# Performance work log

Measured on AMD Instinct MI355X. Metric: run time of the kernel, lower is better.

The kernel has to match this reference:

```python
import jax, jax.numpy as jnp
import numpy as np

B, S, D, H = 2, 2048, 1024, 16
HD = D // H
EPS = 1e-8


def setup_inputs() -> dict:
    key = jax.random.key(0)
    ks = jax.random.split(key, 6)
    x = jax.random.normal(ks[0], (B, S, D), jnp.float32)
    V = jax.random.normal(ks[1], (B, S, H, HD), jnp.float32)
    # binary sparsity mask [B, S, S]
    M = (jax.random.uniform(ks[2], (B, S, S)) > 0.5).astype(jnp.float32)
    # packed QKV in-projection of nn.MultiheadAttention
    in_proj_w = jax.random.normal(ks[3], (3 * D, D), jnp.float32) / np.sqrt(D).astype(np.float32)
    in_proj_b = jnp.zeros((3 * D,), jnp.float32)
    # module-level out_proj (the mha's internal out_proj is discarded)
    out_w = jax.random.normal(ks[4], (D, D), jnp.float32) / np.sqrt(D).astype(np.float32)
    out_b = jnp.zeros((D,), jnp.float32)
    return dict(x=x, V=V, M=M, in_proj_w=in_proj_w, in_proj_b=in_proj_b,
                out_w=out_w, out_b=out_b)


def reference(x, V, M, in_proj_w, in_proj_b, out_w, out_b):
    b, s, d = x.shape
    # packed QKV projection (torch MHA semantics); v-proj computed but its
    # output path (mha output) is discarded by the module, so skip it.
    qkv = x @ in_proj_w.T + in_proj_b              # [B,S,3D]
    q, k, _ = jnp.split(qkv, 3, axis=-1)
    q = q.reshape(b, s, H, HD).transpose(0, 2, 1, 3)   # [B,H,S,HD]
    k = k.reshape(b, s, H, HD).transpose(0, 2, 1, 3)
    scale = np.float32(1.0 / np.sqrt(HD))
    scores = jnp.einsum('bhsd,bhtd->bhst', q, k) * scale  # [B,H,S,S]
    A = jax.nn.softmax(scores, axis=-1)
    # mask + L1 renormalization over keys
    A_sparse = A * M[:, None, :, :]
    norm = jnp.sum(jnp.abs(A_sparse), axis=-1, keepdims=True) + EPS
    A_bar = A_sparse / norm
    # separate value tensor V: [B,S,H,HD] -> [B,H,S,HD]
    Vp = V.transpose(0, 2, 1, 3)
    out = jnp.einsum('bhst,bhtd->bhsd', A_bar, Vp)  # [B,H,S,HD]
    out = out.transpose(0, 2, 1, 3).reshape(b, s, d)
    return out @ out_w.T + out_b
```

## Files before the change

### kernel.cpp

```cpp
#include <hip/hip_runtime.h>
#include <hip/hip_bf16.h>

#define B_  2
#define S_  2048
#define D_  1024
#define H_  16
#define HD_ 64

using bf16x8  = __attribute__((ext_vector_type(8))) __bf16;
using floatx4 = __attribute__((ext_vector_type(4))) float;
using intx4   = __attribute__((ext_vector_type(4))) int;

__device__ __forceinline__ unsigned short f2bf(float f) {
  union { float f; unsigned int i; } v; v.f = f;
  unsigned int r = v.i + 0x7fffu + ((v.i >> 16) & 1u);
  return (unsigned short)(r >> 16);
}
__device__ __forceinline__ unsigned int f2bf_pk(float a, float b) {
  union { __hip_bfloat162 h2; unsigned int u; } c;
  c.h2 = __float22bfloat162_rn(make_float2(a, b));
  return c.u;
}
__device__ __forceinline__ floatx4 mfma16(bf16x8 a, bf16x8 b, floatx4 c) {
  return __builtin_amdgcn_mfma_f32_16x16x32_bf16(a, b, c, 0, 0, 0);
}
__device__ __forceinline__ void gld16(const unsigned short* g, unsigned short* l) {
  __builtin_amdgcn_global_load_lds(
      (const __attribute__((address_space(1))) unsigned int*)g,
      (__attribute__((address_space(3))) unsigned int*)l, 16, 0, 0);
}
#define SW8(row, g) ((((g) ^ ((row) & 7)) * 8))
#define SW4(row, g) ((((g) ^ (((row) >> 1) & 3)) * 8))
#define TAU(r) (((r) & 0x23) | (((r) & 0x08) << 1) | (((r) & 0x04) << 1) | (((r) & 0x10) >> 2))

__global__ __launch_bounds__(256) void prep_kernel(
    const float* __restrict__ x, const float* __restrict__ w_in,
    const float* __restrict__ w_out, const float* __restrict__ V,
    const float* __restrict__ Mm,
    unsigned short* __restrict__ xb, unsigned short* __restrict__ wb,
    unsigned short* __restrict__ wob, unsigned short* __restrict__ vt,
    unsigned long long* __restrict__ mpk)
{
  __shared__ unsigned short tile[64 * 72];
  const int bid = blockIdx.x, tid = threadIdx.x;

  if (bid < 3584) {
    const float* src; unsigned short* dst; int base;
    if (bid < 2048)      { src = x;     dst = xb;  base = bid; }
    else if (bid < 3072) { src = w_in;  dst = wb;  base = bid - 2048; }
    else                 { src = w_out; dst = wob; base = bid - 3072; }
    const int i = (base * 256 + tid) * 8;
    float4 a = *(const float4*)(src + i);
    float4 b = *(const float4*)(src + i + 4);
    union { unsigned int w[4]; intx4 v; } o;
    o.w[0] = f2bf_pk(a.x, a.y); o.w[1] = f2bf_pk(a.z, a.w);
    o.w[2] = f2bf_pk(b.x, b.y); o.w[3] = f2bf_pk(b.z, b.w);
    *(intx4*)(dst + i) = o.v;
  } else if (bid < 5632) {
    const int wave = tid >> 6, lane = tid & 63;
    const int w0 = (bid - 3584) * 64 + wave * 16;
#pragma unroll 4
    for (int j = 0; j < 16; ++j) {
      float v = Mm[(size_t)(w0 + j) * 64 + lane];
      unsigned long long bl = __ballot(v != 0.0f);
      if (lane == 0) mpk[w0 + j] = bl;
    }
  } else {
    const int idx = bid - 5632;
    const int t0 = (idx & 31) * 64, h = (idx >> 5) & 15, b = idx >> 9;
    const int sr = tid >> 3, sc = (tid & 7) * 8;
    const float* src = V + ((size_t)((b * S_ + t0) * H_ + h)) * HD_;
#pragma unroll
    for (int half = 0; half < 2; ++half) {
      const int r = sr + half * 32;
      float4 v0 = *(const float4*)&src[(size_t)r * (H_ * HD_) + sc];
      float4 v1 = *(const float4*)&src[(size_t)r * (H_ * HD_) + sc + 4];
      union { unsigned int w[4]; intx4 v; } p;
      p.w[0] = f2bf_pk(v0.x, v0.y); p.w[1] = f2bf_pk(v0.z, v0.w);
      p.w[2] = f2bf_pk(v1.x, v1.y); p.w[3] = f2bf_pk(v1.z, v1.w);
      *(intx4*)&tile[r * 72 + sc] = p.v;
    }
    __syncthreads();
    unsigned short* dst = vt + ((size_t)((b * H_ + h) * HD_)) * S_ + t0;
    union { unsigned short u[8]; intx4 v; } pack;
#pragma unroll
    for (int j = 0; j < 8; ++j) pack.u[j] = tile[(sc + j) * 72 + sr];
    *(intx4*)&dst[(size_t)sr * S_ + sc] = pack.v;
#pragma unroll
    for (int j = 0; j < 8; ++j) pack.u[j] = tile[(sc + j) * 72 + sr + 32];
    *(intx4*)&dst[(size_t)(sr + 32) * S_ + sc] = pack.v;
  }
}

__global__ __launch_bounds__(256) void gemm_abt(
    const unsigned short* __restrict__ A,
    const unsigned short* __restrict__ Bm,
    const float* __restrict__ bias,
    unsigned short* __restrict__ Cb, float* __restrict__ Cf,
    int M, int N, int K, int qscale)
{
  __shared__ unsigned short As[128 * 32];
  __shared__ unsigned short Bs[128 * 32];

  const int tid  = threadIdx.x;
  const int wave = tid >> 6, lane = tid & 63;
  const int quad = lane >> 4, l15 = lane & 15;
  const int wr = wave >> 1, wc = wave & 1;
  const int bm = blockIdx.y * 128, bn = blockIdx.x * 128;
  const int srow = tid >> 2, gs = tid & 3;

  floatx4 acc[4][4];
#pragma unroll
  for (int mt = 0; mt < 4; ++mt)
#pragma unroll
    for (int nt = 0; nt < 4; ++nt)
      acc[mt][nt] = (floatx4){0.f, 0.f, 0.f, 0.f};

  for (int k0 = 0; k0 < K; k0 += 32) {
    __syncthreads();
#pragma unroll
    for (int r = 0; r < 2; ++r) {
      const int row = srow + r * 64;
      gld16(&A[(size_t)(bm + row) * K + k0 + SW4(row, gs)],
            &As[wave * 512 + r * 2048]);
      gld16(&Bm[(size_t)(bn + row) * K + k0 + SW4(row, gs)],
            &Bs[wave * 512 + r * 2048]);
    }
    __syncthreads();

    bf16x8 af[4], bf[4];
#pragma unroll
    for (int mt = 0; mt < 4; ++mt) {
      const int row = wr * 64 + mt * 16 + l15;
      af[mt] = *(const bf16x8*)&As[row * 32 + SW4(row, quad)];
    }
#pragma unroll
    for (int nt = 0; nt < 4; ++nt) {
      const int row = wc * 64 + nt * 16 + l15;
      bf[nt] = *(const bf16x8*)&Bs[row * 32 + SW4(row, quad)];
    }
#pragma unroll
    for (int mt = 0; mt < 4; ++mt)
#pragma unroll
      for (int nt = 0; nt < 4; ++nt)
        acc[mt][nt] = mfma16(af[mt], bf[nt], acc[mt][nt]);
  }

#pragma unroll
  for (int nt = 0; nt < 4; ++nt) {
    const int col = bn + wc * 64 + nt * 16 + l15;
    const float bi = bias[col];
    const float sc = (qscale && col < 1024) ? 0.125f : 1.0f;
#pragma unroll
    for (int mt = 0; mt < 4; ++mt) {
      const int row0 = bm + wr * 64 + mt * 16 + quad * 4;
#pragma unroll
      for (int reg = 0; reg < 4; ++reg) {
        const float v = (acc[mt][nt][reg] + bi) * sc;
        if (Cf) Cf[(size_t)(row0 + reg) * N + col] = v;
        else    Cb[(size_t)(row0 + reg) * N + col] = f2bf(v);
      }
    }
  }
}

__global__ __launch_bounds__(256) void attn_kernel(
    const unsigned short* __restrict__ QK,
    const unsigned short* __restrict__ Vt,
    const unsigned long long* __restrict__ Mpk,
    unsigned short* __restrict__ ctx)
{
  __shared__ unsigned short Ks[2][64 * 64];
  __shared__ unsigned short Vs[2][64 * 64];
  __shared__ unsigned long long Ms64[2][64];

  const int tid  = threadIdx.x;
  const int wave = tid >> 6, lane = tid & 63;
  const int quad = lane >> 4, l15 = lane & 15;
  const int b = blockIdx.z, h = blockIdx.y, qb = blockIdx.x * 64;
  const int gs = tid & 7;

  const unsigned short* Qbase = QK + (size_t)(b * S_ + qb) * 2048 + h * HD_;
  const unsigned short* Kbase = QK + (size_t)(b * S_) * 2048 + D_ + h * HD_;
  const unsigned short* Vbase = Vt + (size_t)((b * H_ + h) * HD_) * S_;
  const unsigned long long* Mbase = Mpk + (size_t)(b * S_ + qb) * (S_ / 64);

  unsigned short* Qs = &Ks[0][0];
#pragma unroll
  for (int r = 0; r < 2; ++r) {
    const int row = (tid >> 3) + r * 32;
    gld16(Qbase + (size_t)row * 2048 + SW8(row, gs), Qs + wave * 512 + r * 2048);
  }
  if (tid < 64) Ms64[0][tid] = Mbase[(size_t)tid * (S_ / 64)];
  asm volatile("s_waitcnt vmcnt(0)" ::: "memory");
  __syncthreads();

  bf16x8 qf[2];
#pragma unroll
  for (int c = 0; c < 2; ++c) {
    const int row = wave * 16 + l15;
    qf[c] = *(const bf16x8*)&Qs[row * 64 + SW8(row, c * 4 + quad)];
  }
  __syncthreads();

#pragma unroll
  for (int r = 0; r < 2; ++r) {
    const int rowd = (tid >> 3) + r * 32;
    const int tokK = TAU(rowd);
    gld16(Kbase + (size_t)tokK * 2048 + SW8(rowd, gs), &Ks[0][wave * 512 + r * 2048]);
    gld16(Vbase + (size_t)rowd * S_ + SW8(rowd, gs),   &Vs[0][wave * 512 + r * 2048]);
  }

  unsigned int bmask[8];
#pragma unroll
  for (int j = 0; j < 8; ++j) bmask[j] = 1u << (quad * 8 + j);

  floatx4 accO[4];
  float Pp = 0.f;
#pragma unroll
  for (int nt = 0; nt < 4; ++nt)
    accO[nt] = (floatx4){0.f, 0.f, 0.f, 0.f};

  for (int i = 0; i < 32; ++i) {
    const int cur = i & 1, nxt = cur ^ 1;
    asm volatile("s_waitcnt vmcnt(0)" ::: "memory");
    __syncthreads();

    if (i + 1 < 32) {
      const int t1 = (i + 1) * 64;
#pragma unroll
      for (int r = 0; r < 2; ++r) {
        const int rowd = (tid >> 3) + r * 32;
        const int tokK = TAU(rowd);
        gld16(Kbase + (size_t)(t1 + tokK) * 2048 + SW8(rowd, gs),
              &Ks[nxt][wave * 512 + r * 2048]);
        gld16(Vbase + (size_t)rowd * S_ + t1 + SW8(rowd, gs),
              &Vs[nxt][wave * 512 + r * 2048]);
      }
      if (tid < 64)
        Ms64[nxt][tid] = Mbase[(size_t)tid * (S_ / 64) + i + 1];
    }

    floatx4 sc[4];
    __builtin_amdgcn_s_setprio(1);
#pragma unroll
    for (int nt = 0; nt < 4; ++nt) {
      const int row = nt * 16 + l15;
      bf16x8 kf0 = *(const bf16x8*)&Ks[cur][row * 64 + SW8(row, quad)];
      bf16x8 kf1 = *(const bf16x8*)&Ks[cur][row * 64 + SW8(row, 4 + quad)];
      floatx4 z = (floatx4){0.f, 0.f, 0.f, 0.f};
      z = mfma16(kf0, qf[0], z);
      z = mfma16(kf1, qf[1], z);
      sc[nt] = z;
    }
    __builtin_amdgcn_s_setprio(0);

    const unsigned long long mw = Ms64[cur][wave * 16 + l15];

    bf16x8 vf0[4], vf1[4];
#pragma unroll
    for (int nt = 0; nt < 4; ++nt) {
      const int row = nt * 16 + l15;
      vf0[nt] = *(const bf16x8*)&Vs[cur][row * 64 + SW8(row, quad)];
      vf1[nt] = *(const bf16x8*)&Vs[cur][row * 64 + SW8(row, 4 + quad)];
    }

    bf16x8 pa0, pa1;
    {
      const unsigned int mlo = (unsigned int)mw;
      const unsigned int mhi = (unsigned int)(mw >> 32);
      union { unsigned int w[4]; bf16x8 v; } A0, A1;
#pragma unroll
      for (int nt = 0; nt < 4; ++nt) {
        const unsigned int word = (nt < 2) ? mlo : mhi;
        float p[4];
#pragma unroll
        for (int reg = 0; reg < 4; ++reg) {
          const float e = __expf(sc[nt][reg]);
          p[reg] = (word & bmask[(nt & 1) * 4 + reg]) ? e : 0.0f;
        }
        Pp += (p[0] + p[1]) + (p[2] + p[3]);
        const unsigned int d0 = f2bf_pk(p[0], p[1]);
        const unsigned int d1 = f2bf_pk(p[2], p[3]);
        if (nt == 0)      { A0.w[0] = d0; A0.w[1] = d1; }
        else if (nt == 1) { A0.w[2] = d0; A0.w[3] = d1; }
        else if (nt == 2) { A1.w[0] = d0; A1.w[1] = d1; }
        else              { A1.w[2] = d0; A1.w[3] = d1; }
      }
      pa0 = A0.v; pa1 = A1.v;
    }

    __builtin_amdgcn_s_setprio(1);
#pragma unroll
    for (int nt = 0; nt < 4; ++nt) {
      accO[nt] = mfma16(pa0, vf0[nt], accO[nt]);
      accO[nt] = mfma16(pa1, vf1[nt], accO[nt]);
    }
    __builtin_amdgcn_s_setprio(0);
  }

  Pp += __shfl_xor(Pp, 16);
  Pp += __shfl_xor(Pp, 32);
  Pp = 1.0f / (Pp + 1e-30f);
  float Ppe[4];
#pragma unroll
  for (int reg = 0; reg < 4; ++reg)
    Ppe[reg] = __shfl(Pp, (quad << 4) | (quad * 4 + reg));

#pragma unroll
  for (int nt = 0; nt < 4; ++nt)
#pragma unroll
    for (int reg = 0; reg < 4; ++reg) {
      const int row = wave * 16 + quad * 4 + reg;
      ctx[(size_t)(b * S_ + qb + row) * D_ + h * HD_ + nt * 16 + l15] =
          f2bf(accO[nt][reg] * Ppe[reg]);
    }
}

extern "C" void kernel_launch(void* const* d_in, const int* in_sizes, int n_in,
                              void* d_out, int out_size, void* d_ws, size_t ws_size,
                              hipStream_t stream) {
  const float* x     = (const float*)d_in[0];
  const float* V     = (const float*)d_in[1];
  const float* Mm    = (const float*)d_in[2];
  const float* w_in  = (const float*)d_in[3];
  const float* b_in  = (const float*)d_in[4];
  const float* w_out = (const float*)d_in[5];
  const float* b_out = (const float*)d_in[6];
  float* out = (float*)d_out;

  unsigned short* qk  = (unsigned short*)d_ws;
  unsigned short* vt  = qk  + (size_t)8 * 1024 * 1024;
  unsigned short* ctx = vt  + (size_t)4 * 1024 * 1024;
  unsigned short* xb  = ctx + (size_t)4 * 1024 * 1024;
  unsigned short* wb  = xb  + (size_t)4 * 1024 * 1024;
  unsigned short* wob = wb  + (size_t)2 * 1024 * 1024;
  unsigned long long* mpk = (unsigned long long*)(wob + (size_t)1024 * 1024);

  prep_kernel<<<6656, 256, 0, stream>>>(x, w_in, w_out, V, Mm,
                                        xb, wb, wob, vt, mpk);

  gemm_abt<<<dim3(2048 / 128, (B_ * S_) / 128), 256, 0, stream>>>(
      xb, wb, b_in, qk, nullptr, B_ * S_, 2048, D_, 1);

  attn_kernel<<<dim3(S_ / 64, H_, B_), 256, 0, stream>>>(qk, vt, mpk, ctx);

  gemm_abt<<<dim3(D_ / 128, (B_ * S_) / 128), 256, 0, stream>>>(
      ctx, wob, b_out, nullptr, out, B_ * S_, D_, D_, 0);
}
```

Measured before the change: 247.6 us.

## Fold log2e into Q scale, use exp2, and compute row sums via MFMA

Folds log2(e) into the Q projection scale so the attention loop can use the hardware exp2 builtin instead of expf. Masking becomes a sign-extended bitfield AND instead of compare-and-select. Row sums are computed by MFMA against a ones vector instead of scalar adds and end-of-kernel shuffles. Mask words are loaded per lane straight from global memory into registers rather than staged through shared memory, and K/V pointers are advanced incrementally. The row sum now uses the bf16-rounded probabilities, which differ slightly from the fp32 values, and each tile adds two MFMAs.

```diff
diff --git a/kernel.cpp b/kernel.cpp
--- a/kernel.cpp
+++ b/kernel.cpp
@@ -29,9 +29,21 @@
       (const __attribute__((address_space(1))) unsigned int*)g,
       (__attribute__((address_space(3))) unsigned int*)l, 16, 0, 0);
 }
+#if __has_builtin(__builtin_amdgcn_exp2f)
+#define EXP2(x) __builtin_amdgcn_exp2f(x)
+#else
+#define EXP2(x) __expf((x) * 0.6931471805599453f)
+#endif
+#if __has_builtin(__builtin_amdgcn_sbfe)
+#define SBFE1(x, o) __builtin_amdgcn_sbfe((int)(x), (o), 1)
+#else
+#define SBFE1(x, o) (((int)((x) << (31 - (o)))) >> 31)
+#endif
 #define SW8(row, g) ((((g) ^ ((row) & 7)) * 8))
 #define SW4(row, g) ((((g) ^ (((row) >> 1) & 3)) * 8))
 #define TAU(r) (((r) & 0x23) | (((r) & 0x08) << 1) | (((r) & 0x04) << 1) | (((r) & 0x10) >> 2))
+
+#define QSCALE 0.18033688011f
 
 __global__ __launch_bounds__(256) void prep_kernel(
     const float* __restrict__ x, const float* __restrict__ w_in,
@@ -150,7 +162,7 @@
   for (int nt = 0; nt < 4; ++nt) {
     const int col = bn + wc * 64 + nt * 16 + l15;
     const float bi = bias[col];
-    const float sc = (qscale && col < 1024) ? 0.125f : 1.0f;
+    const float sc = (qscale && col < 1024) ? QSCALE : 1.0f;
 #pragma unroll
     for (int mt = 0; mt < 4; ++mt) {
       const int row0 = bm + wr * 64 + mt * 16 + quad * 4;
@@ -172,7 +184,6 @@
 {
   __shared__ unsigned short Ks[2][64 * 64];
   __shared__ unsigned short Vs[2][64 * 64];
-  __shared__ unsigned long long Ms64[2][64];
 
   const int tid  = threadIdx.x;
   const int wave = tid >> 6, lane = tid & 63;
@@ -183,7 +194,8 @@
   const unsigned short* Qbase = QK + (size_t)(b * S_ + qb) * 2048 + h * HD_;
   const unsigned short* Kbase = QK + (size_t)(b * S_) * 2048 + D_ + h * HD_;
   const unsigned short* Vbase = Vt + (size_t)((b * H_ + h) * HD_) * S_;
-  const unsigned long long* Mbase = Mpk + (size_t)(b * S_ + qb) * (S_ / 64);
+  const unsigned long long* Mrow =
+      Mpk + (size_t)(b * S_ + qb + wave * 16 + l15) * (S_ / 64);
 
   unsigned short* Qs = &Ks[0][0];
 #pragma unroll
@@ -191,7 +203,7 @@
     const int row = (tid >> 3) + r * 32;
     gld16(Qbase + (size_t)row * 2048 + SW8(row, gs), Qs + wave * 512 + r * 2048);
   }
-  if (tid < 64) Ms64[0][tid] = Mbase[(size_t)tid * (S_ / 64)];
+  unsigned long long mw_next = Mrow[0];
   asm volatile("s_waitcnt vmcnt(0)" ::: "memory");
   __syncthreads();
 
@@ -203,42 +215,45 @@
   }
   __syncthreads();
 
-#pragma unroll
-  for (int r = 0; r < 2; ++r) {
-    const int rowd = (tid >> 3) + r * 32;
-    const int tokK = TAU(rowd);
-    gld16(Kbase + (size_t)tokK * 2048 + SW8(rowd, gs), &Ks[0][wave * 512 + r * 2048]);
-    gld16(Vbase + (size_t)rowd * S_ + SW8(rowd, gs),   &Vs[0][wave * 512 + r * 2048]);
-  }
-
-  unsigned int bmask[8];
-#pragma unroll
-  for (int j = 0; j < 8; ++j) bmask[j] = 1u << (quad * 8 + j);
+  const int rowd0 = tid >> 3, rowd1 = rowd0 + 32;
+  const unsigned short* kp0 = Kbase + (size_t)TAU(rowd0) * 2048 + SW8(rowd0, gs);
+  const unsigned short* kp1 = Kbase + (size_t)TAU(rowd1) * 2048 + SW8(rowd1, gs);
+  const unsigned short* vp0 = Vbase + (size_t)rowd0 * S_ + SW8(rowd0, gs);
+  const unsigned short* vp1 = Vbase + (size_t)rowd1 * S_ + SW8(rowd1, gs);
+
+  gld16(kp0, &Ks[0][wave * 512]);
+  gld16(kp1, &Ks[0][wave * 512 + 2048]);
+  gld16(vp0, &Vs[0][wave * 512]);
+  gld16(vp1, &Vs[0][wave * 512 + 2048]);
+
+  floatx4 fz = (floatx4){0.f, 0.f, 0.f, 0.f};
+  asm volatile("" : "+v"(fz));
+  union { unsigned int w[4]; bf16x8 v; } onesU;
+  onesU.w[0] = onesU.w[1] = onesU.w[2] = onesU.w[3] = 0x3F803F80u;
+  bf16x8 ones = onesU.v;
+  asm volatile("" : "+v"(ones));
 
   floatx4 accO[4];
-  float Pp = 0.f;
-#pragma unroll
-  for (int nt = 0; nt < 4; ++nt)
-    accO[nt] = (floatx4){0.f, 0.f, 0.f, 0.f};
+  floatx4 accP = fz;
+#pragma unroll
+  for (int nt = 0; nt < 4; ++nt) accO[nt] = fz;
+
+  const int q8 = quad * 8;
 
   for (int i = 0; i < 32; ++i) {
     const int cur = i & 1, nxt = cur ^ 1;
     asm volatile("s_waitcnt vmcnt(0)" ::: "memory");
     __syncthreads();
 
+    const unsigned long long mw = mw_next;
+
     if (i + 1 < 32) {
-      const int t1 = (i + 1) * 64;
-#pragma unroll
-      for (int r = 0; r < 2; ++r) {
-        const int rowd = (tid >> 3) + r * 32;
-        const int tokK = TAU(rowd);
-        gld16(Kbase + (size_t)(t1 + tokK) * 2048 + SW8(rowd, gs),
-              &Ks[nxt][wave * 512 + r * 2048]);
-        gld16(Vbase + (size_t)rowd * S_ + t1 + SW8(rowd, gs),
-              &Vs[nxt][wave * 512 + r * 2048]);
-      }
-      if (tid < 64)
-        Ms64[nxt][tid] = Mbase[(size_t)tid * (S_ / 64) + i + 1];
+      kp0 += 64 * 2048; kp1 += 64 * 2048; vp0 += 64; vp1 += 64;
+      gld16(kp0, &Ks[nxt][wave * 512]);
+      gld16(kp1, &Ks[nxt][wave * 512 + 2048]);
+      gld16(vp0, &Vs[nxt][wave * 512]);
+      gld16(vp1, &Vs[nxt][wave * 512 + 2048]);
+      mw_next = Mrow[i + 1];
     }
 
     floatx4 sc[4];
@@ -248,14 +263,11 @@
       const int row = nt * 16 + l15;
       bf16x8 kf0 = *(const bf16x8*)&Ks[cur][row * 64 + SW8(row, quad)];
       bf16x8 kf1 = *(const bf16x8*)&Ks[cur][row * 64 + SW8(row, 4 + quad)];
-      floatx4 z = (floatx4){0.f, 0.f, 0.f, 0.f};
-      z = mfma16(kf0, qf[0], z);
+      floatx4 z = mfma16(kf0, qf[0], fz);
       z = mfma16(kf1, qf[1], z);
       sc[nt] = z;
     }
     __builtin_amdgcn_s_setprio(0);
-
-    const unsigned long long mw = Ms64[cur][wave * 16 + l15];
 
     bf16x8 vf0[4], vf1[4];
 #pragma unroll
@@ -265,21 +277,22 @@
       vf1[nt] = *(const bf16x8*)&Vs[cur][row * 64 + SW8(row, 4 + quad)];
     }
 
+    const unsigned int w_lo = ((unsigned int)mw) >> q8;
+    const unsigned int w_hi = ((unsigned int)(mw >> 32)) >> q8;
     bf16x8 pa0, pa1;
     {
-      const unsigned int mlo = (unsigned int)mw;
-      const unsigned int mhi = (unsigned int)(mw >> 32);
       union { unsigned int w[4]; bf16x8 v; } A0, A1;
 #pragma unroll
       for (int nt = 0; nt < 4; ++nt) {
-        const unsigned int word = (nt < 2) ? mlo : mhi;
+        const unsigned int ws = (nt < 2) ? w_lo : w_hi;
         float p[4];
 #pragma unroll
         for (int reg = 0; reg < 4; ++reg) {
-          const float e = __expf(sc[nt][reg]);
-          p[reg] = (word & bmask[(nt & 1) * 4 + reg]) ? e : 0.0f;
+          const int j = (nt & 1) * 4 + reg;
+          const float e = EXP2(sc[nt][reg]);
+          const int m = SBFE1(ws, j);
+          p[reg] = __uint_as_float(__float_as_uint(e) & (unsigned int)m);
         }
-        Pp += (p[0] + p[1]) + (p[2] + p[3]);
         const unsigned int d0 = f2bf_pk(p[0], p[1]);
         const unsigned int d1 = f2bf_pk(p[2], p[3]);
         if (nt == 0)      { A0.w[0] = d0; A0.w[1] = d1; }
@@ -291,6 +304,8 @@
     }
 
     __builtin_amdgcn_s_setprio(1);
+    accP = mfma16(pa0, ones, accP);
+    accP = mfma16(pa1, ones, accP);
 #pragma unroll
     for (int nt = 0; nt < 4; ++nt) {
       accO[nt] = mfma16(pa0, vf0[nt], accO[nt]);
@@ -299,13 +314,10 @@
     __builtin_amdgcn_s_setprio(0);
   }
 
-  Pp += __shfl_xor(Pp, 16);
-  Pp += __shfl_xor(Pp, 32);
-  Pp = 1.0f / (Pp + 1e-30f);
   float Ppe[4];
 #pragma unroll
   for (int reg = 0; reg < 4; ++reg)
-    Ppe[reg] = __shfl(Pp, (quad << 4) | (quad * 4 + reg));
+    Ppe[reg] = 1.0f / (accP[reg] + 1e-30f);
 
 #pragma unroll
   for (int nt = 0; nt < 4; ++nt)
```

Result: slower. 261.6 us (+5.7%).
